# Kernel tuning notes

Measured on AMD Instinct MI355X. Metric: run time of the kernel, lower is better.

## Reference

```python
import jax, jax.numpy as jnp
import numpy as np

B, N, C, NUM_HEADS, POOL = 8, 3136, 768, 12, 3
HIDDEN = 4 * C
EPS = 1e-5


def setup_inputs() -> dict:
    key = jax.random.key(0)
    ks = jax.random.split(key, 6)
    g = lambda k, shape, sc: (jax.random.normal(k, shape, jnp.float32) * sc)
    return {
        "x": g(ks[0], (B, N, C), 1.0),
        "ln1_g": jnp.ones((C,), jnp.float32),
        "ln1_b": jnp.zeros((C,), jnp.float32),
        "qkv_w": g(ks[1], (3 * C, C), 0.02),
        "proj_w": g(ks[2], (C, C), 0.02),
        "proj_b": jnp.zeros((C,), jnp.float32),
        "ln2_g": jnp.ones((C,), jnp.float32),
        "ln2_b": jnp.zeros((C,), jnp.float32),
        "fc1_w": g(ks[3], (HIDDEN, C), 0.02),
        "fc1_b": jnp.zeros((HIDDEN,), jnp.float32),
        "fc2_w": g(ks[4], (C, HIDDEN), 0.02),
        "fc2_b": jnp.zeros((C,), jnp.float32),
    }


def _ln(z, g, b):
    m = jnp.mean(z, axis=-1, keepdims=True)
    v = jnp.var(z, axis=-1, keepdims=True)
    return (z - m) * jax.lax.rsqrt(v + EPS) * g + b


def _avgpool_seq(t):
    # t: (B, H, N, hd); AvgPool1d(kernel=3, stride=3, pad=1, count_include_pad=True)
    s = jax.lax.reduce_window(
        t, jnp.float32(0), jax.lax.add,
        window_dimensions=(1, 1, POOL, 1),
        window_strides=(1, 1, POOL, 1),
        padding=((0, 0), (0, 0), (POOL // 2, POOL // 2), (0, 0)),
    )
    return s / POOL


def reference(x, ln1_g, ln1_b, qkv_w, proj_w, proj_b, ln2_g, ln2_b, fc1_w, fc1_b, fc2_w, fc2_b):
    b, n, c = x.shape
    hd = c // NUM_HEADS
    # --- attention sublayer ---
    h = _ln(x, ln1_g, ln1_b)
    qkv = (h @ qkv_w.T).reshape(b, n, 3, NUM_HEADS, hd).transpose(2, 0, 3, 1, 4)
    q, k, v = qkv[0], qkv[1], qkv[2]  # each (B, H, N, hd)
    k = _avgpool_seq(k)  # (B, H, Np, hd)
    v = _avgpool_seq(v)
    attn = jnp.einsum('bhqd,bhkd->bhqk', q, k) * (hd ** -0.5)
    attn = jax.nn.softmax(attn, axis=-1)
    o = jnp.einsum('bhqk,bhkd->bhqd', attn, v)
    o = o.transpose(0, 2, 1, 3).reshape(b, n, c)
    x = x + (o @ proj_w.T + proj_b)
    # --- MLP sublayer ---
    h2 = _ln(x, ln2_g, ln2_b)
    m = jax.nn.gelu(h2 @ fc1_w.T + fc1_b, approximate=False)
    m = m @ fc2_w.T + fc2_b
    return x + m
```

## Files before the change

### kernel.cpp

```cpp
#include <hip/hip_runtime.h>
#include <hip/hip_bf16.h>
#include <math.h>

#define B_   8
#define N_   3136
#define C_   768
#define H_   12
#define HD_  64
#define NP_  1046
#define NPP_ 1056
#define M_   (B_*N_)
#define MKV_ (B_*NPP_)

typedef __bf16 bf16x8 __attribute__((ext_vector_type(8)));
typedef float  f32x4  __attribute__((ext_vector_type(4)));

__device__ __forceinline__ float bf2f(__hip_bfloat16 v){ return __bfloat162float(v); }
__device__ __forceinline__ __hip_bfloat16 f2bf(float v){ return __float2bfloat16(v); }

__device__ __forceinline__ void load_lds16(const void* g, void* l) {
  __builtin_amdgcn_global_load_lds(
      (const __attribute__((address_space(1))) unsigned int*)g,
      (__attribute__((address_space(3))) unsigned int*)l, 16, 0, 0);
}

#define MFMA16(a,b,c) __builtin_amdgcn_mfma_f32_16x16x32_bf16((a),(b),(c),0,0,0)

__device__ __forceinline__ float gelu_f(float v) {
  float y = 1.5957691f * (v + 0.044715f * v * v * v);
  float e = __expf(y);
  return v * e / (e + 1.0f);
}

__global__ void cvt_kernel(const float* __restrict__ s0, __hip_bfloat16* __restrict__ d0, int n0,
                           const float* __restrict__ s1, __hip_bfloat16* __restrict__ d1, int n1,
                           const float* __restrict__ s2, __hip_bfloat16* __restrict__ d2, int n2,
                           const float* __restrict__ s3, __hip_bfloat16* __restrict__ d3, int n3) {
  int i = blockIdx.x * 256 + threadIdx.x;
  if (i < n0) d0[i] = f2bf(s0[i]);
  i -= n0;
  if (i >= 0 && i < n1) d1[i] = f2bf(s1[i]);
  i -= n1;
  if (i >= 0 && i < n2) d2[i] = f2bf(s2[i]);
  i -= n2;
  if (i >= 0 && i < n3) d3[i] = f2bf(s3[i]);
}

__global__ __launch_bounds__(256)
void ln_kernel(const float* __restrict__ x, const float* __restrict__ g,
               const float* __restrict__ bta, __hip_bfloat16* __restrict__ out) {
  const size_t row = blockIdx.x;
  const float* xr = x + row * C_;
  const int t = threadIdx.x;
  float v0 = xr[t], v1 = xr[t + 256], v2 = xr[t + 512];
  float s  = v0 + v1 + v2;
  float s2 = v0*v0 + v1*v1 + v2*v2;
  #pragma unroll
  for (int off = 32; off > 0; off >>= 1) { s += __shfl_down(s, off); s2 += __shfl_down(s2, off); }
  __shared__ float ws1[4], ws2[4];
  if ((t & 63) == 0) { ws1[t >> 6] = s; ws2[t >> 6] = s2; }
  __syncthreads();
  float S  = ws1[0] + ws1[1] + ws1[2] + ws1[3];
  float S2 = ws2[0] + ws2[1] + ws2[2] + ws2[3];
  float mean = S * (1.0f / C_);
  float var  = S2 * (1.0f / C_) - mean * mean;
  float rstd = rsqrtf(var + 1e-5f);
  __hip_bfloat16* orow = out + row * C_;
  orow[t]       = f2bf((v0 - mean) * rstd * g[t]       + bta[t]);
  orow[t + 256] = f2bf((v1 - mean) * rstd * g[t + 256] + bta[t + 256]);
  orow[t + 512] = f2bf((v2 - mean) * rstd * g[t + 512] + bta[t + 512]);
}

__global__ void pool_h_kernel(const __hip_bfloat16* __restrict__ h, __hip_bfloat16* __restrict__ hp) {
  int idx = blockIdx.x * 256 + threadIdx.x;
  int c  = idx % C_;
  int np = (idx / C_) % NPP_;
  int b  = idx / (C_ * NPP_);
  float a = 0.f;
  if (np < NP_) {
    #pragma unroll
    for (int t = 0; t < 3; ++t) {
      int n = np * 3 - 1 + t;
      if (n >= 0 && n < N_) a += bf2f(h[((size_t)b * N_ + n) * C_ + c]);
    }
    a *= (1.0f / 3.0f);
  }
  hp[idx] = f2bf(a);
}

__global__ __launch_bounds__(256)
void rearr_kernel(const __hip_bfloat16* __restrict__ kv,
                  __hip_bfloat16* __restrict__ kp, __hip_bfloat16* __restrict__ vpt) {
  __shared__ __align__(16) __hip_bfloat16 sk[32][64], sv[32][64];
  const int bh = blockIdx.y;
  const int b = bh / H_, h = bh % H_;
  const int np0 = blockIdx.x * 32;
  const int t = threadIdx.x;
  const int nl = t >> 3, d8 = (t & 7) * 8;
  const __hip_bfloat16* src = kv + ((size_t)(b * NPP_) + np0 + nl) * 1536 + h * 64;
  *(bf16x8*)&sk[nl][d8] = *(const bf16x8*)(src + d8);
  *(bf16x8*)&sv[nl][d8] = *(const bf16x8*)(src + 768 + d8);
  __syncthreads();
  {
    int lhi = nl >> 3, rr = nl & 7;
    int p = (rr < 4) ? (lhi * 4 + rr) : (16 + lhi * 4 + rr - 4);
    *(bf16x8*)(kp + ((size_t)bh * NPP_ + np0 + p) * 64 + d8) = *(const bf16x8*)&sk[nl][d8];
  }
  {
    int d = t >> 2, n8 = (t & 3) * 8;
    bf16x8 v;
    #pragma unroll
    for (int j = 0; j < 8; ++j) v[j] = sv[n8 + j][d];
    *(bf16x8*)(vpt + ((size_t)bh * 64 + d) * NPP_ + np0 + n8) = v;
  }
}

__global__ __launch_bounds__(256)
void attn_kernel(const __hip_bfloat16* __restrict__ qb,
                 const __hip_bfloat16* __restrict__ kp,
                 const __hip_bfloat16* __restrict__ vpt,
                 __hip_bfloat16* __restrict__ o) {
  __shared__ __align__(16) char smem[16384];
  const int tid  = threadIdx.x;
  const int lane = tid & 63;
  const int w    = tid >> 6;
  const int bh = blockIdx.y;
  const int b = bh / H_, h = bh % H_;
  const int q0 = blockIdx.x * 128 + w * 32;
  const int l15 = lane & 15, lhi = lane >> 4;

  bf16x8 qf[2][2];
  #pragma unroll
  for (int f = 0; f < 2; ++f) {
    int qrow = q0 + f * 16 + l15;
    if (qrow >= N_) qrow = N_ - 1;
    const __hip_bfloat16* qptr = qb + ((size_t)(b * N_ + qrow)) * C_ + h * HD_ + lhi * 8;
    qf[f][0] = *(const bf16x8*)(qptr);
    qf[f][1] = *(const bf16x8*)(qptr + 32);
    #pragma unroll
    for (int i = 0; i < 8; ++i) {
      qf[f][0][i] = qf[f][0][i] * (__bf16)0.125f;
      qf[f][1][i] = qf[f][1][i] * (__bf16)0.125f;
    }
  }

  const char* kp_base  = (const char*)(kp  + (size_t)bh * NPP_ * HD_);
  const char* vpt_base = (const char*)(vpt + (size_t)bh * HD_ * NPP_);
  const int krow_s = tid >> 3;
  const int pK = (tid & 7) * 16;
  const int srcKoff = krow_s * 128 + (pK ^ ((krow_s & 7) << 4));
  const int qV = pK ^ ((krow_s & 7) << 4);
  const int vrow_s = 2 * krow_s + (qV >> 6);
  const int srcVoff = vrow_s * (NPP_ * 2) + (qV & 63);

  char* dstK[2] = { smem + 0    + w * 1024, smem + 8192 + 0    + w * 1024 };
  char* dstV[2] = { smem + 4096 + w * 1024, smem + 8192 + 4096 + w * 1024 };

  load_lds16(kp_base + srcKoff, dstK[0]);
  load_lds16(vpt_base + srcVoff, dstV[0]);
  __syncthreads();

  f32x4 oacc[2][4] = {};
  float lp[2] = {0.f, 0.f};

  for (int kc = 0; kc < NPP_; kc += 32) {
    const int cur = (kc >> 5) & 1;
    if (kc + 32 < NPP_) {
      load_lds16(kp_base + (size_t)(kc + 32) * 128 + srcKoff, dstK[cur ^ 1]);
      load_lds16(vpt_base + (size_t)(kc + 32) * 2 + srcVoff, dstV[cur ^ 1]);
    }
    const char* sK = smem + cur * 8192;
    const char* sV = smem + cur * 8192 + 4096;

    bf16x8 ka0 = *(const bf16x8*)(sK + l15 * 128        + (( 0 + 16 * lhi) ^ ((l15 & 7) << 4)));
    bf16x8 ka1 = *(const bf16x8*)(sK + l15 * 128        + ((64 + 16 * lhi) ^ ((l15 & 7) << 4)));
    bf16x8 kb0 = *(const bf16x8*)(sK + (16 + l15) * 128 + (( 0 + 16 * lhi) ^ ((l15 & 7) << 4)));
    bf16x8 kb1 = *(const bf16x8*)(sK + (16 + l15) * 128 + ((64 + 16 * lhi) ^ ((l15 & 7) << 4)));
    bf16x8 vf[4];
    #pragma unroll
    for (int nb = 0; nb < 4; ++nb) {
      int row = nb * 16 + l15;
      int Lv = row >> 1;
      int p = (((row & 1) * 64) + 16 * lhi) ^ ((Lv & 7) << 4);
      vf[nb] = *(const bf16x8*)(sV + Lv * 128 + p);
    }

    #pragma unroll
    for (int f = 0; f < 2; ++f) {
      f32x4 s0 = {}, s1 = {};
      s0 = MFMA16(ka0, qf[f][0], s0);
      s0 = MFMA16(ka1, qf[f][1], s0);
      s1 = MFMA16(kb0, qf[f][0], s1);
      s1 = MFMA16(kb1, qf[f][1], s1);
      bf16x8 pa;
      #pragma unroll
      for (int r = 0; r < 4; ++r) {
        float p0 = (kc + lhi * 8 + r     < NP_) ? __expf(s0[r]) : 0.f;
        float p1 = (kc + lhi * 8 + 4 + r < NP_) ? __expf(s1[r]) : 0.f;
        lp[f] += p0 + p1;
        pa[r]     = (__bf16)p0;
        pa[r + 4] = (__bf16)p1;
      }
      #pragma unroll
      for (int nb = 0; nb < 4; ++nb)
        oacc[f][nb] = MFMA16(pa, vf[nb], oacc[f][nb]);
    }
    __syncthreads();
  }

  #pragma unroll
  for (int f = 0; f < 2; ++f) {
    float lpf = lp[f];
    lpf += __shfl_xor(lpf, 16);
    lpf += __shfl_xor(lpf, 32);
    #pragma unroll
    for (int r = 0; r < 4; ++r) {
      int orow = q0 + f * 16 + lhi * 4 + r;
      if (orow < N_) {
        float inv = 1.0f / __shfl(lpf, lhi * 4 + r);
        size_t rowbase = ((size_t)(b * N_ + orow)) * C_ + h * HD_;
        #pragma unroll
        for (int nb = 0; nb < 4; ++nb)
          o[rowbase + nb * 16 + l15] = f2bf(oacc[f][nb][r] * inv);
      }
    }
  }
}

__global__ __launch_bounds__(256, 2)
void gemm128(const __hip_bfloat16* __restrict__ A,
             const __hip_bfloat16* __restrict__ Bt,
             const float* __restrict__ bias,
             const float* __restrict__ res, float* __restrict__ out,
             int M, int N, int K) {
  __shared__ __align__(16) __hip_bfloat16 sA[4][128 * 32];
  __shared__ __align__(16) __hip_bfloat16 sB[4][128 * 32];
  const int tid = threadIdx.x, lane = tid & 63, wid = tid >> 6;
  const int wr = wid >> 1, wc = wid & 1;
  const int l15 = lane & 15, lhi = lane >> 4;

  const int nwg = gridDim.x;
  const int ntx = N >> 7;
  const int qq = nwg >> 3, rr8 = nwg & 7;
  const int xcd = blockIdx.x & 7, off8 = blockIdx.x >> 3;
  const int wg = (xcd < rr8 ? xcd * (qq + 1) : rr8 * (qq + 1) + (xcd - rr8) * qq) + off8;
  const long row0 = (long)(wg / ntx) * 128;
  const long col0 = (long)(wg % ntx) * 128;

  const size_t ldb = (size_t)K * 2;
  const int R = tid >> 2;
  const int scol = ((tid & 3) * 16) ^ ((R & 3) << 4);
  const char* gA = (const char*)A  + (size_t)(row0 + R) * ldb + scol;
  const char* gB = (const char*)Bt + (size_t)(col0 + R) * ldb + scol;

  const int fsw = (lhi * 16) ^ ((l15 & 3) << 4);

  f32x4 acc[4][4] = {};

#define STG(b, t) { \
    const char* ga_ = gA + (size_t)(t) * 64; \
    const char* gb_ = gB + (size_t)(t) * 64; \
    char* la_ = (char*)&sA[b][0] + wid * 1024; \
    char* lb_ = (char*)&sB[b][0] + wid * 1024; \
    load_lds16(ga_, la_); \
    load_lds16(ga_ + 64 * ldb, la_ + 4096); \
    load_lds16(gb_, lb_); \
    load_lds16(gb_ + 64 * ldb, lb_ + 4096); }

  const int NT = K >> 5;
  STG(0, 0); STG(1, 1); STG(2, 2);
  asm volatile("s_waitcnt vmcnt(8)" ::: "memory");
  __syncthreads();

  for (int t = 0; t < NT; ++t) {
    const int b = t & 3;
    bf16x8 af[4], bfv[4];
    const char* pa_ = (const char*)&sA[b][0] + (wr * 64 + l15) * 64 + fsw;
    const char* pb_ = (const char*)&sB[b][0] + (wc * 64 + l15) * 64 + fsw;
    #pragma unroll
    for (int m = 0; m < 4; ++m) af[m]  = *(const bf16x8*)(pa_ + m * 16 * 64);
    #pragma unroll
    for (int n = 0; n < 4; ++n) bfv[n] = *(const bf16x8*)(pb_ + n * 16 * 64);
    if (t + 3 < NT) {
      STG((t + 3) & 3, t + 3);
      asm volatile("s_waitcnt vmcnt(8)" ::: "memory");
    } else if (t + 2 < NT) {
      asm volatile("s_waitcnt vmcnt(4)" ::: "memory");
    } else if (t + 1 < NT) {
      asm volatile("s_waitcnt vmcnt(0)" ::: "memory");
    }
    __builtin_amdgcn_sched_barrier(0);
    __builtin_amdgcn_s_barrier();
    __builtin_amdgcn_sched_barrier(0);
    __builtin_amdgcn_s_setprio(1);
    #pragma unroll
    for (int m = 0; m < 4; ++m)
      #pragma unroll
      for (int n = 0; n < 4; ++n)
        acc[m][n] = MFMA16(af[m], bfv[n], acc[m][n]);
    __builtin_amdgcn_s_setprio(0);
  }
#undef STG

  #pragma unroll
  for (int m = 0; m < 4; ++m) {
    long rbase = row0 + wr * 64 + m * 16 + lhi * 4;
    #pragma unroll
    for (int n = 0; n < 4; ++n) {
      long col = col0 + wc * 64 + n * 16 + l15;
      #pragma unroll
      for (int r = 0; r < 4; ++r) {
        size_t idx = (size_t)(rbase + r) * N + col;
        out[idx] = acc[m][n][r] + bias[col] + res[idx];
      }
    }
  }
}

__global__ __launch_bounds__(256, 2)
void gemm128b(const __hip_bfloat16* __restrict__ A,
              const __hip_bfloat16* __restrict__ Bt,
              __hip_bfloat16* __restrict__ out,
              int M, int N, int K) {
  __shared__ __align__(16) __hip_bfloat16 sA[4][128 * 32];
  __shared__ __align__(16) __hip_bfloat16 sB[4][128 * 32];
  const int tid = threadIdx.x, lane = tid & 63, wid = tid >> 6;
  const int wr = wid >> 1, wc = wid & 1;
  const int l15 = lane & 15, lhi = lane >> 4;

  const int nwg = gridDim.x;
  const int ntx = N >> 7;
  const int qq = nwg >> 3, rr8 = nwg & 7;
  const int xcd = blockIdx.x & 7, off8 = blockIdx.x >> 3;
  const int wg = (xcd < rr8 ? xcd * (qq + 1) : rr8 * (qq + 1) + (xcd - rr8) * qq) + off8;
  const long row0 = (long)(wg / ntx) * 128;
  const long col0 = (long)(wg % ntx) * 128;

  const size_t ldb = (size_t)K * 2;
  const int R = tid >> 2;
  const int scol = ((tid & 3) * 16) ^ ((R & 3) << 4);
  const char* gA = (const char*)A  + (size_t)(row0 + R) * ldb + scol;
  const char* gB = (const char*)Bt + (size_t)(col0 + R) * ldb + scol;

  const int fsw = (lhi * 16) ^ ((l15 & 3) << 4);

  f32x4 acc[4][4] = {};

#define STG(b, t) { \
    const char* ga_ = gA + (size_t)(t) * 64; \
    const char* gb_ = gB + (size_t)(t) * 64; \
    char* la_ = (char*)&sA[b][0] + wid * 1024; \
    char* lb_ = (char*)&sB[b][0] + wid * 1024; \
    load_lds16(ga_, la_); \
    load_lds16(ga_ + 64 * ldb, la_ + 4096); \
    load_lds16(gb_, lb_); \
    load_lds16(gb_ + 64 * ldb, lb_ + 4096); }

  const int NT = K >> 5;
  STG(0, 0); STG(1, 1); STG(2, 2);
  asm volatile("s_waitcnt vmcnt(8)" ::: "memory");
  __syncthreads();

  for (int t = 0; t < NT; ++t) {
    const int b = t & 3;
    bf16x8 af[4], bfv[4];
    const char* pa_ = (const char*)&sA[b][0] + (wr * 64 + l15) * 64 + fsw;
    const char* pb_ = (const char*)&sB[b][0] + (wc * 64 + l15) * 64 + fsw;
    #pragma unroll
    for (int m = 0; m < 4; ++m) af[m]  = *(const bf16x8*)(pa_ + m * 16 * 64);
    #pragma unroll
    for (int n = 0; n < 4; ++n) bfv[n] = *(const bf16x8*)(pb_ + n * 16 * 64);
    if (t + 3 < NT) {
      STG((t + 3) & 3, t + 3);
      asm volatile("s_waitcnt vmcnt(8)" ::: "memory");
    } else if (t + 2 < NT) {
      asm volatile("s_waitcnt vmcnt(4)" ::: "memory");
    } else if (t + 1 < NT) {
      asm volatile("s_waitcnt vmcnt(0)" ::: "memory");
    }
    __builtin_amdgcn_sched_barrier(0);
    __builtin_amdgcn_s_barrier();
    __builtin_amdgcn_sched_barrier(0);
    __builtin_amdgcn_s_setprio(1);
    #pragma unroll
    for (int m = 0; m < 4; ++m)
      #pragma unroll
      for (int n = 0; n < 4; ++n)
        acc[m][n] = MFMA16(af[m], bfv[n], acc[m][n]);
    __builtin_amdgcn_s_setprio(0);
  }
#undef STG

  #pragma unroll
  for (int m = 0; m < 4; ++m) {
    long rbase = row0 + wr * 64 + m * 16 + lhi * 4;
    #pragma unroll
    for (int n = 0; n < 4; ++n) {
      long col = col0 + wc * 64 + n * 16 + l15;
      #pragma unroll
      for (int r = 0; r < 4; ++r) {
        size_t idx = (size_t)(rbase + r) * N + col;
        out[idx] = f2bf(acc[m][n][r]);
      }
    }
  }
}

template<int EPI>
__global__ __launch_bounds__(512, 2)
void gemm256(const __hip_bfloat16* __restrict__ A,
             const __hip_bfloat16* __restrict__ Bt,
             const float* __restrict__ bias,
             const float* res, void* outv,
             int M, int N, int K) {
  extern __shared__ __align__(16) char lds[];
  const int tid = threadIdx.x;
  const int lane = tid & 63;
  const int wid = tid >> 6;
  const int wr = wid >> 2;
  const int wc = wid & 3;
  const int l15 = lane & 15, lhi = lane >> 4;

  const int nwg = gridDim.x;
  const int ntx = N >> 8;
  const int qq = nwg >> 3, rr8 = nwg & 7;
  const int xcd = blockIdx.x & 7, off8 = blockIdx.x >> 3;
  const int wg = (xcd < rr8 ? xcd * (qq + 1) : rr8 * (qq + 1) + (xcd - rr8) * qq) + off8;
  const long row0 = (long)(wg / ntx) * 256;
  const long col0 = (long)(wg % ntx) * 256;

  const size_t ldb = (size_t)K * 2;
  const int srow = wid * 16 + (lane >> 2);
  const int scol = ((lane & 3) * 16) ^ (lane & 32);
  const char* gA = (const char*)A  + (size_t)(row0 + srow) * ldb + scol;
  const char* gB = (const char*)Bt + (size_t)(col0 + srow) * ldb + scol;

#define STAGEH(op, t, kh, bb) { \
    const char* g_ = (op ? gB : gA) + (size_t)(t) * 128 + (kh) * 64; \
    char* l_ = lds + ((op) ? 65536 : 0) + (bb) * 32768 + (kh) * 16384 + wid * 1024; \
    load_lds16(g_, l_); \
    load_lds16(g_ + 128 * ldb, l_ + 8192); \
  }

  const int fragswz = (lhi * 16) ^ ((l15 & 8) << 2);
  const char* ldsA = lds + wr * 8192 + l15 * 64 + fragswz;
  const char* ldsB = lds + 65536 + wc * 4096 + l15 * 64 + fragswz;

  f32x4 acc[8][4] = {};
  bf16x8 bfr[4];

#define VM4 asm volatile("s_waitcnt vmcnt(4)" ::: "memory")
#define SBAR() { __builtin_amdgcn_sched_barrier(0); __builtin_amdgcn_s_barrier(); __builtin_amdgcn_sched_barrier(0); }

#define PHASE(bb, ks, mq, STG, VM) { \
    const char* pA_ = ldsA + (bb) * 32768 + (ks) * 16384 + (mq) * 4096; \
    bf16x8 afr[4]; \
    _Pragma("unroll") for (int i_ = 0; i_ < 4; ++i_) afr[i_] = *(const bf16x8*)(pA_ + i_ * 1024); \
    if ((mq) == 0) { \
      const char* pB_ = ldsB + (bb) * 32768 + (ks) * 16384; \
      _Pragma("unroll") for (int j_ = 0; j_ < 4; ++j_) bfr[j_] = *(const bf16x8*)(pB_ + j_ * 1024); \
    } \
    STG; \
    VM; \
    SBAR(); \
    __builtin_amdgcn_s_setprio(1); \
    _Pragma("unroll") for (int i_ = 0; i_ < 4; ++i_) \
      _Pragma("unroll") for (int j_ = 0; j_ < 4; ++j_) \
        acc[(mq) * 4 + i_][j_] = MFMA16(afr[i_], bfr[j_], acc[(mq) * 4 + i_][j_]); \
    __builtin_amdgcn_s_setprio(0); \
    SBAR(); \
  }

  STAGEH(0, 0, 0, 0); STAGEH(1, 0, 0, 0);
  STAGEH(0, 0, 1, 0); STAGEH(1, 0, 1, 0);
  STAGEH(0, 1, 0, 1); STAGEH(1, 1, 0, 1);
  VM4;
  SBAR();

  const int NT = K >> 6;
  for (int it = 0; it < (NT >> 1); ++it) {
    const int u = 2 * it;
    const bool s2 = (u + 2) < NT, s3 = (u + 3) < NT;
    PHASE(0, 0, 0, STAGEH(0, u + 1, 1, 1), );
    PHASE(0, 0, 1, STAGEH(1, u + 1, 1, 1), );
    PHASE(0, 1, 0, if (s2) STAGEH(0, u + 2, 0, 0), );
    PHASE(0, 1, 1, if (s2) STAGEH(1, u + 2, 0, 0), VM4);
    PHASE(1, 0, 0, if (s2) STAGEH(0, u + 2, 1, 0), );
    PHASE(1, 0, 1, if (s2) STAGEH(1, u + 2, 1, 0), );
    PHASE(1, 1, 0, if (s3) STAGEH(0, u + 3, 0, 1), );
    PHASE(1, 1, 1, if (s3) STAGEH(1, u + 3, 0, 1), VM4);
  }
#undef PHASE
#undef STAGEH
#undef VM4
#undef SBAR

  #pragma unroll
  for (int mf = 0; mf < 8; ++mf) {
    long rbase = row0 + wr * 128 + mf * 16 + lhi * 4;
    #pragma unroll
    for (int nf = 0; nf < 4; ++nf) {
      long col = col0 + wc * 64 + nf * 16 + l15;
      #pragma unroll
      for (int r = 0; r < 4; ++r) {
        size_t idx = (size_t)(rbase + r) * N + col;
        float v = acc[mf][nf][r];
        if (EPI == 0) {
          ((__hip_bfloat16*)outv)[idx] = f2bf(v);
        } else if (EPI == 1) {
          ((float*)outv)[idx] = v + bias[col] + res[idx];
        } else {
          ((__hip_bfloat16*)outv)[idx] = f2bf(gelu_f(v + bias[col]));
        }
      }
    }
  }
}

extern "C" void kernel_launch(void* const* d_in, const int* in_sizes, int n_in,
                              void* d_out, int out_size, void* d_ws, size_t ws_size,
                              hipStream_t stream) {
  const float* x      = (const float*)d_in[0];
  const float* ln1_g  = (const float*)d_in[1];
  const float* ln1_b  = (const float*)d_in[2];
  const float* qkv_w  = (const float*)d_in[3];
  const float* proj_w = (const float*)d_in[4];
  const float* proj_b = (const float*)d_in[5];
  const float* ln2_g  = (const float*)d_in[6];
  const float* ln2_b  = (const float*)d_in[7];
  const float* fc1_w  = (const float*)d_in[8];
  const float* fc1_b  = (const float*)d_in[9];
  const float* fc2_w  = (const float*)d_in[10];
  const float* fc2_b  = (const float*)d_in[11];
  float* out = (float*)d_out;

  char* ws = (char*)d_ws;
  __hip_bfloat16* wqkv  = (__hip_bfloat16*)(ws + 0);
  __hip_bfloat16* wproj = (__hip_bfloat16*)(ws + 3538944);
  __hip_bfloat16* wfc1  = (__hip_bfloat16*)(ws + 4718592);
  __hip_bfloat16* wfc2  = (__hip_bfloat16*)(ws + 9437184);
  __hip_bfloat16* hbuf  = (__hip_bfloat16*)(ws + 14155776);
  __hip_bfloat16* obuf  = (__hip_bfloat16*)(ws + 52690944);
  __hip_bfloat16* kpb   = (__hip_bfloat16*)(ws + 91226112);
  __hip_bfloat16* vptb  = (__hip_bfloat16*)(ws + 104202240);
  __hip_bfloat16* big   = (__hip_bfloat16*)(ws + 117178368);
  const size_t WS_NEEDED = 117178368ull + 154140672ull;
  if (ws_size < WS_NEEDED) return;

  __hip_bfloat16* qb   = big;
  __hip_bfloat16* kvb  = (__hip_bfloat16*)((char*)big + 38535168);
  __hip_bfloat16* hp   = (__hip_bfloat16*)((char*)big + 64487424);

  hipFuncSetAttribute((const void*)gemm256<2>, hipFuncAttributeMaxDynamicSharedMemorySize, 131072);

  {
    int n0 = 2304 * 768, n1 = 768 * 768, n2 = 3072 * 768, n3 = 768 * 3072;
    int tot = n0 + n1 + n2 + n3;
    cvt_kernel<<<(tot + 255) / 256, 256, 0, stream>>>(qkv_w, wqkv, n0, proj_w, wproj, n1,
                                                      fc1_w, wfc1, n2, fc2_w, wfc2, n3);
  }

  ln_kernel<<<M_, 256, 0, stream>>>(x, ln1_g, ln1_b, hbuf);
  gemm128b<<<(M_ / 128) * (768 / 128), 256, 0, stream>>>(hbuf, wqkv, qb, M_, 768, 768);
  pool_h_kernel<<<(B_ * NPP_ * C_) / 256, 256, 0, stream>>>(hbuf, hp);
  gemm128b<<<(MKV_ / 128) * (1536 / 128), 256, 0, stream>>>(hp, wqkv + 768 * 768, kvb, MKV_, 1536, 768);
  rearr_kernel<<<dim3(NPP_ / 32, B_ * H_), 256, 0, stream>>>(kvb, kpb, vptb);
  attn_kernel<<<dim3((N_ + 127) / 128, B_ * H_), 256, 0, stream>>>(qb, kpb, vptb, obuf);
  gemm128<<<(M_ / 128) * (768 / 128), 256, 0, stream>>>(obuf, wproj, proj_b, x, out, M_, 768, 768);

  ln_kernel<<<M_, 256, 0, stream>>>(out, ln2_g, ln2_b, hbuf);
  gemm256<2><<<(M_ / 256) * (3072 / 256), 512, 131072, stream>>>(hbuf, wfc1, fc1_b, nullptr, big, M_, 3072, 768);
  gemm128<<<(M_ / 128) * (768 / 128), 256, 0, stream>>>(big, wfc2, fc2_b, out, out, M_, 768, 3072);
}
```

Before: 700.5 us.

## Replace 256x256 fc1 GEMM with 128x128 four-stage pipelined tile kernel; vectorize weight cast

The fc1 GEMM moves from a 512-thread 256x256 tile kernel with 128KB dynamic LDS to a 256-thread 128x128 tile kernel. The new kernel uses a 4-deep LDS ring buffer with K-step 32 and direct global-to-LDS loads, and fuses bias plus GELU into its epilogue. The aim is better occupancy and more workgroups for the grid, at the cost of less data reuse per tile and more global traffic. Separately, the weight conversion kernel now handles four floats per thread with vector loads and stores.

```diff
diff --git a/kernel.cpp b/kernel.cpp
--- a/kernel.cpp
+++ b/kernel.cpp
@@ -32,18 +32,23 @@
   return v * e / (e + 1.0f);
 }
 
-__global__ void cvt_kernel(const float* __restrict__ s0, __hip_bfloat16* __restrict__ d0, int n0,
-                           const float* __restrict__ s1, __hip_bfloat16* __restrict__ d1, int n1,
-                           const float* __restrict__ s2, __hip_bfloat16* __restrict__ d2, int n2,
-                           const float* __restrict__ s3, __hip_bfloat16* __restrict__ d3, int n3) {
+__device__ __forceinline__ void cvt4(const float* __restrict__ s, __hip_bfloat16* __restrict__ d, int i4) {
+  float4 v = *(const float4*)(s + i4);
+  __hip_bfloat16 o[4] = { f2bf(v.x), f2bf(v.y), f2bf(v.z), f2bf(v.w) };
+  *(short4*)(d + i4) = *(const short4*)o;
+}
+__global__ void cvt_kernel(const float* __restrict__ s0, __hip_bfloat16* __restrict__ d0, int q0,
+                           const float* __restrict__ s1, __hip_bfloat16* __restrict__ d1, int q1,
+                           const float* __restrict__ s2, __hip_bfloat16* __restrict__ d2, int q2,
+                           const float* __restrict__ s3, __hip_bfloat16* __restrict__ d3, int q3) {
   int i = blockIdx.x * 256 + threadIdx.x;
-  if (i < n0) d0[i] = f2bf(s0[i]);
-  i -= n0;
-  if (i >= 0 && i < n1) d1[i] = f2bf(s1[i]);
-  i -= n1;
-  if (i >= 0 && i < n2) d2[i] = f2bf(s2[i]);
-  i -= n2;
-  if (i >= 0 && i < n3) d3[i] = f2bf(s3[i]);
+  if (i < q0) { cvt4(s0, d0, i * 4); return; }
+  i -= q0;
+  if (i < q1) { cvt4(s1, d1, i * 4); return; }
+  i -= q1;
+  if (i < q2) { cvt4(s2, d2, i * 4); return; }
+  i -= q2;
+  if (i < q3) { cvt4(s3, d3, i * 4); }
 }
 
 __global__ __launch_bounds__(256)
@@ -406,112 +411,91 @@
   }
 }
 
-template<int EPI>
-__global__ __launch_bounds__(512, 2)
-void gemm256(const __hip_bfloat16* __restrict__ A,
-             const __hip_bfloat16* __restrict__ Bt,
-             const float* __restrict__ bias,
-             const float* res, void* outv,
-             int M, int N, int K) {
-  extern __shared__ __align__(16) char lds[];
-  const int tid = threadIdx.x;
-  const int lane = tid & 63;
-  const int wid = tid >> 6;
-  const int wr = wid >> 2;
-  const int wc = wid & 3;
+__global__ __launch_bounds__(256, 2)
+void gemm128g(const __hip_bfloat16* __restrict__ A,
+              const __hip_bfloat16* __restrict__ Bt,
+              const float* __restrict__ bias,
+              __hip_bfloat16* __restrict__ out,
+              int M, int N, int K) {
+  __shared__ __align__(16) __hip_bfloat16 sA[4][128 * 32];
+  __shared__ __align__(16) __hip_bfloat16 sB[4][128 * 32];
+  const int tid = threadIdx.x, lane = tid & 63, wid = tid >> 6;
+  const int wr = wid >> 1, wc = wid & 1;
   const int l15 = lane & 15, lhi = lane >> 4;
 
   const int nwg = gridDim.x;
-  const int ntx = N >> 8;
+  const int ntx = N >> 7;
   const int qq = nwg >> 3, rr8 = nwg & 7;
   const int xcd = blockIdx.x & 7, off8 = blockIdx.x >> 3;
   const int wg = (xcd < rr8 ? xcd * (qq + 1) : rr8 * (qq + 1) + (xcd - rr8) * qq) + off8;
-  const long row0 = (long)(wg / ntx) * 256;
-  const long col0 = (long)(wg % ntx) * 256;
+  const long row0 = (long)(wg / ntx) * 128;
+  const long col0 = (long)(wg % ntx) * 128;
 
   const size_t ldb = (size_t)K * 2;
-  const int srow = wid * 16 + (lane >> 2);
-  const int scol = ((lane & 3) * 16) ^ (lane & 32);
-  const char* gA = (const char*)A  + (size_t)(row0 + srow) * ldb + scol;
-  const char* gB = (const char*)Bt + (size_t)(col0 + srow) * ldb + scol;
-
-#define STAGEH(op, t, kh, bb) { \
-    const char* g_ = (op ? gB : gA) + (size_t)(t) * 128 + (kh) * 64; \
-    char* l_ = lds + ((op) ? 65536 : 0) + (bb) * 32768 + (kh) * 16384 + wid * 1024; \
-    load_lds16(g_, l_); \
-    load_lds16(g_ + 128 * ldb, l_ + 8192); \
-  }
-
-  const int fragswz = (lhi * 16) ^ ((l15 & 8) << 2);
-  const char* ldsA = lds + wr * 8192 + l15 * 64 + fragswz;
-  const char* ldsB = lds + 65536 + wc * 4096 + l15 * 64 + fragswz;
-
-  f32x4 acc[8][4] = {};
-  bf16x8 bfr[4];
-
-#define VM4 asm volatile("s_waitcnt vmcnt(4)" ::: "memory")
-#define SBAR() { __builtin_amdgcn_sched_barrier(0); __builtin_amdgcn_s_barrier(); __builtin_amdgcn_sched_barrier(0); }
-
-#define PHASE(bb, ks, mq, STG, VM) { \
-    const char* pA_ = ldsA + (bb) * 32768 + (ks) * 16384 + (mq) * 4096; \
-    bf16x8 afr[4]; \
-    _Pragma("unroll") for (int i_ = 0; i_ < 4; ++i_) afr[i_] = *(const bf16x8*)(pA_ + i_ * 1024); \
-    if ((mq) == 0) { \
-      const char* pB_ = ldsB + (bb) * 32768 + (ks) * 16384; \
-      _Pragma("unroll") for (int j_ = 0; j_ < 4; ++j_) bfr[j_] = *(const bf16x8*)(pB_ + j_ * 1024); \
-    } \
-    STG; \
-    VM; \
-    SBAR(); \
-    __builtin_amdgcn_s_setprio(1); \
-    _Pragma("unroll") for (int i_ = 0; i_ < 4; ++i_) \
-      _Pragma("unroll") for (int j_ = 0; j_ < 4; ++j_) \
-        acc[(mq) * 4 + i_][j_] = MFMA16(afr[i_], bfr[j_], acc[(mq) * 4 + i_][j_]); \
-    __builtin_amdgcn_s_setprio(0); \
-    SBAR(); \
-  }
-
-  STAGEH(0, 0, 0, 0); STAGEH(1, 0, 0, 0);
-  STAGEH(0, 0, 1, 0); STAGEH(1, 0, 1, 0);
-  STAGEH(0, 1, 0, 1); STAGEH(1, 1, 0, 1);
-  VM4;
-  SBAR();
-
-  const int NT = K >> 6;
-  for (int it = 0; it < (NT >> 1); ++it) {
-    const int u = 2 * it;
-    const bool s2 = (u + 2) < NT, s3 = (u + 3) < NT;
-    PHASE(0, 0, 0, STAGEH(0, u + 1, 1, 1), );
-    PHASE(0, 0, 1, STAGEH(1, u + 1, 1, 1), );
-    PHASE(0, 1, 0, if (s2) STAGEH(0, u + 2, 0, 0), );
-    PHASE(0, 1, 1, if (s2) STAGEH(1, u + 2, 0, 0), VM4);
-    PHASE(1, 0, 0, if (s2) STAGEH(0, u + 2, 1, 0), );
-    PHASE(1, 0, 1, if (s2) STAGEH(1, u + 2, 1, 0), );
-    PHASE(1, 1, 0, if (s3) STAGEH(0, u + 3, 0, 1), );
-    PHASE(1, 1, 1, if (s3) STAGEH(1, u + 3, 0, 1), VM4);
-  }
-#undef PHASE
-#undef STAGEH
-#undef VM4
-#undef SBAR
+  const int R = tid >> 2;
+  const int scol = ((tid & 3) * 16) ^ ((R & 3) << 4);
+  const char* gA = (const char*)A  + (size_t)(row0 + R) * ldb + scol;
+  const char* gB = (const char*)Bt + (size_t)(col0 + R) * ldb + scol;
+
+  const int fsw = (lhi * 16) ^ ((l15 & 3) << 4);
+
+  f32x4 acc[4][4] = {};
+
+#define STG(b, t) { \
+    const char* ga_ = gA + (size_t)(t) * 64; \
+    const char* gb_ = gB + (size_t)(t) * 64; \
+    char* la_ = (char*)&sA[b][0] + wid * 1024; \
+    char* lb_ = (char*)&sB[b][0] + wid * 1024; \
+    load_lds16(ga_, la_); \
+    load_lds16(ga_ + 64 * ldb, la_ + 4096); \
+    load_lds16(gb_, lb_); \
+    load_lds16(gb_ + 64 * ldb, lb_ + 4096); }
+
+  const int NT = K >> 5;
+  STG(0, 0); STG(1, 1); STG(2, 2);
+  asm volatile("s_waitcnt vmcnt(8)" ::: "memory");
+  __syncthreads();
+
+  for (int t = 0; t < NT; ++t) {
+    const int b = t & 3;
+    bf16x8 af[4], bfv[4];
+    const char* pa_ = (const char*)&sA[b][0] + (wr * 64 + l15) * 64 + fsw;
+    const char* pb_ = (const char*)&sB[b][0] + (wc * 64 + l15) * 64 + fsw;
+    #pragma unroll
+    for (int m = 0; m < 4; ++m) af[m]  = *(const bf16x8*)(pa_ + m * 16 * 64);
+    #pragma unroll
+    for (int n = 0; n < 4; ++n) bfv[n] = *(const bf16x8*)(pb_ + n * 16 * 64);
+    if (t + 3 < NT) {
+      STG((t + 3) & 3, t + 3);
+      asm volatile("s_waitcnt vmcnt(8)" ::: "memory");
+    } else if (t + 2 < NT) {
+      asm volatile("s_waitcnt vmcnt(4)" ::: "memory");
+    } else if (t + 1 < NT) {
+      asm volatile("s_waitcnt vmcnt(0)" ::: "memory");
+    }
+    __builtin_amdgcn_sched_barrier(0);
+    __builtin_amdgcn_s_barrier();
+    __builtin_amdgcn_sched_barrier(0);
+    __builtin_amdgcn_s_setprio(1);
+    #pragma unroll
+    for (int m = 0; m < 4; ++m)
+      #pragma unroll
+      for (int n = 0; n < 4; ++n)
+        acc[m][n] = MFMA16(af[m], bfv[n], acc[m][n]);
+    __builtin_amdgcn_s_setprio(0);
+  }
+#undef STG
 
   #pragma unroll
-  for (int mf = 0; mf < 8; ++mf) {
-    long rbase = row0 + wr * 128 + mf * 16 + lhi * 4;
-    #pragma unroll
-    for (int nf = 0; nf < 4; ++nf) {
-      long col = col0 + wc * 64 + nf * 16 + l15;
+  for (int m = 0; m < 4; ++m) {
+    long rbase = row0 + wr * 64 + m * 16 + lhi * 4;
+    #pragma unroll
+    for (int n = 0; n < 4; ++n) {
+      long col = col0 + wc * 64 + n * 16 + l15;
       #pragma unroll
       for (int r = 0; r < 4; ++r) {
         size_t idx = (size_t)(rbase + r) * N + col;
-        float v = acc[mf][nf][r];
-        if (EPI == 0) {
-          ((__hip_bfloat16*)outv)[idx] = f2bf(v);
-        } else if (EPI == 1) {
-          ((float*)outv)[idx] = v + bias[col] + res[idx];
-        } else {
-          ((__hip_bfloat16*)outv)[idx] = f2bf(gelu_f(v + bias[col]));
-        }
+        out[idx] = f2bf(gelu_f(acc[m][n][r] + bias[col]));
       }
     }
   }
@@ -551,13 +535,11 @@
   __hip_bfloat16* kvb  = (__hip_bfloat16*)((char*)big + 38535168);
   __hip_bfloat16* hp   = (__hip_bfloat16*)((char*)big + 64487424);
 
-  hipFuncSetAttribute((const void*)gemm256<2>, hipFuncAttributeMaxDynamicSharedMemorySize, 131072);
-
   {
-    int n0 = 2304 * 768, n1 = 768 * 768, n2 = 3072 * 768, n3 = 768 * 3072;
-    int tot = n0 + n1 + n2 + n3;
-    cvt_kernel<<<(tot + 255) / 256, 256, 0, stream>>>(qkv_w, wqkv, n0, proj_w, wproj, n1,
-                                                      fc1_w, wfc1, n2, fc2_w, wfc2, n3);
+    int q0 = (2304 * 768) / 4, q1 = (768 * 768) / 4, q2 = (3072 * 768) / 4, q3 = (768 * 3072) / 4;
+    int tot = q0 + q1 + q2 + q3;
+    cvt_kernel<<<(tot + 255) / 256, 256, 0, stream>>>(qkv_w, wqkv, q0, proj_w, wproj, q1,
+                                                      fc1_w, wfc1, q2, fc2_w, wfc2, q3);
   }
 
   ln_kernel<<<M_, 256, 0, stream>>>(x, ln1_g, ln1_b, hbuf);
@@ -569,6 +551,6 @@
   gemm128<<<(M_ / 128) * (768 / 128), 256, 0, stream>>>(obuf, wproj, proj_b, x, out, M_, 768, 768);
 
   ln_kernel<<<M_, 256, 0, stream>>>(out, ln2_g, ln2_b, hbuf);
-  gemm256<2><<<(M_ / 256) * (3072 / 256), 512, 131072, stream>>>(hbuf, wfc1, fc1_b, nullptr, big, M_, 3072, 768);
+  gemm128g<<<(M_ / 128) * (3072 / 128), 256, 0, stream>>>(hbuf, wfc1, fc1_b, big, M_, 3072, 768);
   gemm128<<<(M_ / 128) * (768 / 128), 256, 0, stream>>>(big, wfc2, fc2_b, out, out, M_, 768, 3072);
 }
```

New measurement: 684.9 us (median of 2 runs). -2.2%, faster.
